# Optimization experiments

Measured on AMD Instinct MI355X. Metric: run time of the kernel, lower is better.

The kernel has to match this reference:

```python
import jax, jax.numpy as jnp
import numpy as np

# Geometry constants matching __init__ defaults
DG = 2        # deformable_groups
KS = 3        # kernel_size
K = KS * KS   # taps per kernel
DIL = 2       # dilation
PAD = 2       # padding = dilation
STRIDE = 1


def setup_inputs() -> dict:
    key = jax.random.key(0)
    k1, k2, k3, k4 = jax.random.split(key, 4)
    B, C, H, W = 4, 128, 96, 192
    Cout = 128
    x = jax.random.normal(k1, (B, C, H, W), dtype=jnp.float32)
    # offset/mask conv: grouped conv, groups=DG -> in-channels per group = C//DG
    off_out = DG * 3 * K  # 54 (36 offset + 18 mask)
    # small weights so learned offsets are O(1) pixels (realistic trained regime;
    # the original zero-init would make the gather trivial)
    w_offset = jax.random.normal(k2, (off_out, C // DG, KS, KS), dtype=jnp.float32) * 0.01
    b_offset = jax.random.normal(k3, (off_out,), dtype=jnp.float32) * 0.1
    stdv = 1.0 / np.sqrt(C * KS * KS)
    w_deform = jax.random.uniform(k4, (Cout, C, KS, KS), dtype=jnp.float32,
                                  minval=-stdv, maxval=stdv)
    return {"x": x, "w_offset": w_offset, "b_offset": b_offset, "w_deform": w_deform}


def _deform_conv2d(x, w_offset, b_offset, w_deform):
    B, C, H, W = x.shape
    Cout = w_deform.shape[0]
    Cg = C // DG
    # --- offset/mask conv (grouped, dilated) ---
    om = jax.lax.conv_general_dilated(
        x, w_offset, (STRIDE, STRIDE), [(PAD, PAD), (PAD, PAD)],
        rhs_dilation=(DIL, DIL), feature_group_count=DG,
        dimension_numbers=("NCHW", "OIHW", "NCHW"))
    om = om + b_offset[None, :, None, None]
    Ho, Wo = om.shape[2], om.shape[3]
    off_ch = DG * 2 * K
    offset = om[:, :off_ch]                       # [B, 36, Ho, Wo]
    mask = jax.nn.sigmoid(om[:, off_ch:]) * 2.0   # double_mask=True -> *2
    # torchvision layout: channel 2*(g*K+k) = dy, +1 = dx
    off = offset.reshape(B, DG, K, 2, Ho, Wo)
    m = mask.reshape(B, DG, K, Ho, Wo)
    # --- sampling coordinates ---
    ky = (jnp.arange(K) // KS).astype(x.dtype)
    kx = (jnp.arange(K) % KS).astype(x.dtype)
    base_y = (jnp.arange(Ho) * STRIDE - PAD).astype(x.dtype)
    base_x = (jnp.arange(Wo) * STRIDE - PAD).astype(x.dtype)
    py = base_y[None, None, None, :, None] + (ky * DIL)[None, None, :, None, None] + off[:, :, :, 0]
    px = base_x[None, None, None, None, :] + (kx * DIL)[None, None, :, None, None] + off[:, :, :, 1]
    y0 = jnp.floor(py)
    x0 = jnp.floor(px)
    ty = py - y0
    tx = px - x0
    xflat = x.reshape(B, DG, Cg, H * W)
    # gather[b,g,c,n] = xflat[b,g,c, idx[b,g,n]]
    gather = jax.vmap(jax.vmap(lambda xg, idx: jnp.take(xg, idx, axis=1)))
    val = jnp.zeros((B, DG, Cg, K, Ho, Wo), x.dtype)
    # accumulate bilinear corners one at a time to bound peak memory
    for dy, dx, wgt in ((0, 0, (1 - ty) * (1 - tx)), (0, 1, (1 - ty) * tx),
                        (1, 0, ty * (1 - tx)), (1, 1, ty * tx)):
        yy = y0 + dy
        xx = x0 + dx
        valid = (yy >= 0) & (yy < H) & (xx >= 0) & (xx < W)
        yc = jnp.clip(yy, 0, H - 1).astype(jnp.int32)
        xc = jnp.clip(xx, 0, W - 1).astype(jnp.int32)
        lin = (yc * W + xc).reshape(B, DG, K * Ho * Wo)
        g = gather(xflat, lin).reshape(B, DG, Cg, K, Ho, Wo)
        val = val + jnp.where(valid, wgt, 0.0)[:, :, None] * g
    val = val * m[:, :, None]  # modulation mask per deformable group / tap
    wr = w_deform.reshape(Cout, DG, Cg, K)
    return jnp.einsum("ogck,bgckhw->bohw", wr, val)


def reference(x, w_offset, b_offset, w_deform):
    return _deform_conv2d(x, w_offset, b_offset, w_deform)
```

## Files before the change

kernel.cpp:

```cpp
#include <hip/hip_runtime.h>
#include <hip/hip_fp16.h>
#include <math.h>

#define BB   4
#define C_   128
#define H_   96
#define W_   192
#define COUT 128
#define DG_  2
#define CG_  64
#define K_   9
#define HO   96
#define WO   192
#define HW   (H_ * W_)
#define OMCH 54
#define RDIM (C_ * K_)
#define NKS  (RDIM / 32)
#define CSTEP 2
#define NCH  (NKS / CSTEP)
#define VROW 18

typedef __attribute__((ext_vector_type(8))) _Float16 f16x8;
typedef __attribute__((ext_vector_type(4))) float f32x4;

static __device__ __forceinline__ ushort f2bf(float f) {
  union { float f; uint u; } v; v.f = f;
  uint r = v.u + 0x7fff + ((v.u >> 16) & 1);
  return (ushort)(r >> 16);
}

__global__ __launch_bounds__(256) void prep_k(
    const float* __restrict__ wd, const float* __restrict__ wo,
    ushort* __restrict__ WtA, ushort* __restrict__ Awo2) {
  int i = blockIdx.x * 256 + threadIdx.x;
  if (i < 128 * RDIM) {
    int blkA = i >> 9, within = i & 511;
    int oct = within >> 7, colA = (within >> 3) & 15, j = within & 7;
    int m = blkA & 1, wvq = (blkA >> 1) & 3, s = blkA >> 3;
    int o = wvq * 32 + m * 16 + colA;
    int r = s * 32 + oct * 8 + j;
    int g = r / 576, t = r - g * 576;
    int k = t >> 6, cg = t & 63;
    WtA[i] = __half_as_ushort(__float2half(wd[((size_t)o * C_ + g * 64 + cg) * 9 + k]));
  }
  if (i < 64 * RDIM) {
    int blkA = i >> 9, within = i & 511;
    int oct = within >> 7, colA = (within >> 3) & 15, j = within & 7;
    int wv2 = blkA & 3, s = blkA >> 2;
    int o2 = wv2 * 16 + colA;
    int r = s * 32 + oct * 8 + j;
    int g = r / 576, t = r - g * 576;
    int k = t >> 6, cg = t & 63;
    int g2 = o2 >> 5, j2 = o2 & 31;
    float v = ((g2 == g) && (j2 < 27))
                ? wo[(((size_t)(g2 * 27 + j2)) * 64 + cg) * 9 + k] : 0.f;
    Awo2[i] = __half_as_ushort(__float2half(v));
  }
}

__global__ __launch_bounds__(256) void xt_k(
    const float* __restrict__ x, __half* __restrict__ xT) {
  __shared__ float t[128][65];
  int blk = blockIdx.x;
  int b = blk / 288, p0 = (blk % 288) * 64;
  int q = threadIdx.x >> 6, l = threadIdx.x & 63;
  const float* xb = x + (size_t)b * C_ * HW;
#pragma unroll
  for (int it = 0; it < 32; ++it) {
    int c = q * 32 + it;
    t[c][l] = xb[(size_t)c * HW + p0 + l];
  }
  __syncthreads();
  uint* xTb = (uint*)(xT + (size_t)b * HW * 128);
#pragma unroll
  for (int it = 0; it < 16; ++it) {
    int px = q * 16 + it;
    union { __half2 h; uint u; } pk;
    pk.h = __half2{__float2half(t[2 * l][px]), __float2half(t[2 * l + 1][px])};
    xTb[(size_t)(p0 + px) * 64 + l] = pk.u;
  }
}

__global__ __launch_bounds__(256, 6) void offset_nhwc_k(
    const __half* __restrict__ xT, const ushort* __restrict__ Awo2,
    const float* __restrict__ b_offset, float* __restrict__ om) {
  __shared__ uint s_val[2][CSTEP * 64 * VROW];

  int bid = blockIdx.x;
  int blk = (bid & 7) * 144 + (bid >> 3);
  int wt = blk % 3, bh = blk / 3;
  int ho = bh % HO, b = bh / HO;
  int wo0 = wt * 64;
  int tid = threadIdx.x;
  int lane = tid & 63, wv = tid >> 6;
  int sub = lane >> 3, q = lane & 7;
  int col = lane & 15, oct = lane >> 4;

  const __half* xTb = xT + (size_t)b * HW * 128;

  f32x4 acc[4];
#pragma unroll
  for (int n = 0; n < 4; ++n) acc[n] = (f32x4){0.f, 0.f, 0.f, 0.f};

  uint4 C0[2];
  uint  MK[2];
  int   IX[2];

  auto issue_chunk = [&](int c) {
#pragma unroll
    for (int t = 0; t < 2; ++t) {
      int po = wv * 2 + t;
      int gk = c;
      int px = po * 8 + sub;
      int g = gk >= 9, k = gk - 9 * g;
      int dy = k / 3, dx = k - dy * 3;
      int y  = ho - 2 + 2 * dy;
      int xc = wo0 + px - 2 + 2 * dx;
      bool ok = (y >= 0) & (y < H_) & (xc >= 0) & (xc < W_);
      int yc  = min(max(y, 0), H_ - 1);
      int xcc = min(max(xc, 0), W_ - 1);
      const __half* p = xTb + (size_t)(yc * W_ + xcc) * 128 + g * 64 + q * 8;
      C0[t] = *(const uint4*)(p);
      MK[t] = ok ? 0x3c003c00u : 0u;
      int step_local = q >> 2;
      IX[t] = (step_local * 64 + px) * VROW + (q & 3) * 4;
    }
  };

  auto finish_chunk = [&](int nb) {
#pragma unroll
    for (int t = 0; t < 2; ++t) {
      union { __half2 h2; uint u; } m; m.u = MK[t];
      uint res[4];
      const uint* a = (const uint*)&C0[t];
#pragma unroll
      for (int h = 0; h < 4; ++h) {
        union { __half2 h2; uint u; } p, vv;
        p.u = a[h];
        vv.h2 = __hmul2(p.h2, m.h2);
        res[h] = vv.u;
      }
      *(uint4*)&s_val[nb][IX[t]] = make_uint4(res[0], res[1], res[2], res[3]);
    }
  };

  auto mfma_chunk = [&](int c, int cb) {
#pragma unroll
    for (int ls = 0; ls < CSTEP; ++ls) {
      int s = c * CSTEP + ls;
      const ushort* ab = Awo2 + (size_t)(s * 4 + wv) * 512 + (oct * 16 + col) * 8;
      f16x8 a0 = *(const f16x8*)(ab);
#pragma unroll
      for (int n = 0; n < 4; ++n) {
        f16x8 bfr = *(const f16x8*)
            &s_val[cb][(ls * 64 + n * 16 + col) * VROW + oct * 4];
        acc[n] = __builtin_amdgcn_mfma_f32_16x16x32_f16(a0, bfr, acc[n], 0, 0, 0);
      }
    }
  };

  issue_chunk(0);
  finish_chunk(0);
  __syncthreads();

  for (int c = 0; c < NCH; ++c) {
    if (c < NCH - 1) issue_chunk(c + 1);
    mfma_chunk(c, c & 1);
    if (c < NCH - 1) finish_chunk((c + 1) & 1);
    __syncthreads();
  }

#pragma unroll
  for (int n = 0; n < 4; ++n)
#pragma unroll
    for (int ri = 0; ri < 4; ++ri) {
      int o2 = wv * 16 + oct * 4 + ri;
      int g = o2 >> 5, j = o2 & 31;
      if (j < 27) {
        int ch = g * 27 + j;
        om[((size_t)(b * OMCH + ch) * HO + ho) * WO + wo0 + n * 16 + col] =
            acc[n][ri] + b_offset[ch];
      }
    }
}

__global__ __launch_bounds__(256, 4) void deform_main_k(
    const __half* __restrict__ xT, const float* __restrict__ om,
    const ushort* __restrict__ WtA, float* __restrict__ out) {
  __shared__ uint  s_addr[18 * 64];
  __shared__ uint2 s_wq[18 * 64];
  __shared__ uint  s_val[2][CSTEP * 64 * VROW];

  int bid = blockIdx.x;
  int blk = (bid & 7) * 144 + (bid >> 3);
  int wt = blk % 3, bh = blk / 3;
  int ho = bh % HO, b = bh / HO;
  int wo0 = wt * 64;
  int tid = threadIdx.x;
  int lane = tid & 63, wv = tid >> 6;

  for (int e = tid; e < 18 * 64; e += 256) {
    int px = e & 63, gk = e >> 6;
    int g = gk / 9, k = gk - g * 9;
    int wo = wo0 + px;
    const float* omb = om + (size_t)b * OMCH * HW + (size_t)ho * WO + wo;
    float offy = omb[(size_t)(g * 18 + k * 2 + 0) * HW];
    float offx = omb[(size_t)(g * 18 + k * 2 + 1) * HW];
    float z    = omb[(size_t)(36 + g * 9 + k) * HW];
    float msk  = 2.f / (1.f + __expf(-z));
    float py = (float)(ho - 2 + (k / 3) * 2) + offy;
    float px_ = (float)(wo - 2 + (k % 3) * 2) + offx;
    float y0f = floorf(py), x0f = floorf(px_);
    int   y0 = (int)y0f, x0 = (int)x0f;
    float ty = py - y0f, tx = px_ - x0f;
    float wy0 = (y0 >= 0 && y0 < H_)      ? (1.f - ty) : 0.f;
    float wy1 = (y0 >= -1 && y0 < H_ - 1) ? ty         : 0.f;
    float wx0 = (x0 >= 0 && x0 < W_)      ? (1.f - tx) : 0.f;
    float wx1 = (x0 >= -1 && x0 < W_ - 1) ? tx         : 0.f;
    int yb  = min(max(y0, 0), H_ - 2);
    int xb_ = min(max(x0, 0), W_ - 2);
    float wAy = (y0 == yb      ? wy0 : 0.f) + (y0 + 1 == yb      ? wy1 : 0.f);
    float wBy = (y0 == yb + 1  ? wy0 : 0.f) + (y0 + 1 == yb + 1  ? wy1 : 0.f);
    float wAx = (x0 == xb_     ? wx0 : 0.f) + (x0 + 1 == xb_     ? wx1 : 0.f);
    float wBx = (x0 == xb_ + 1 ? wx0 : 0.f) + (x0 + 1 == xb_ + 1 ? wx1 : 0.f);
    s_addr[e] = (uint)((yb * W_ + xb_) * 128);
    union { __half2 h; uint u; } uA, uB;
    uA.h = __half2{__float2half(wAy * wAx * msk), __float2half(wAy * wBx * msk)};
    uB.h = __half2{__float2half(wBy * wAx * msk), __float2half(wBy * wBx * msk)};
    s_wq[e] = make_uint2(uA.u, uB.u);
  }

  const __half* xTb = xT + (size_t)b * HW * 128;
  int sub = lane >> 3, q = lane & 7;
  int col = lane & 15, oct = lane >> 4;

  f32x4 acc[2][4];
#pragma unroll
  for (int m = 0; m < 2; ++m)
#pragma unroll
    for (int n = 0; n < 4; ++n) acc[m][n] = (f32x4){0.f, 0.f, 0.f, 0.f};

  uint4 C0[2], C1[2], C2[2], C3[2];
  uint2 WQ[2];
  int   IX[2];

  auto issue_chunk = [&](int c) {
#pragma unroll
    for (int t = 0; t < 2; ++t) {
      int po = wv * 2 + t;
      int gk = c;
      int px = po * 8 + sub;
      int ci = gk * 64 + px;
      uint base = s_addr[ci];
      WQ[t] = s_wq[ci];
      int g = gk >= 9;
      const __half* p = xTb + base + g * 64 + q * 8;
      C0[t] = *(const uint4*)(p);
      C1[t] = *(const uint4*)(p + 128);
      C2[t] = *(const uint4*)(p + W_ * 128);
      C3[t] = *(const uint4*)(p + W_ * 128 + 128);
      int step_local = q >> 2;
      int row = step_local * 64 + px;
      IX[t] = row * VROW + (q & 3) * 4;
    }
  };

  auto finish_chunk = [&](int nb) {
#pragma unroll
    for (int t = 0; t < 2; ++t) {
      union { __half2 h; uint u; } w0, w1;
      w0.u = WQ[t].x; w1.u = WQ[t].y;
      __half2 wAx = __low2half2(w0.h), wAy = __high2half2(w0.h);
      __half2 wBx = __low2half2(w1.h), wBy = __high2half2(w1.h);
      uint res[4];
      const uint* a  = (const uint*)&C0[t];
      const uint* b1 = (const uint*)&C1[t];
      const uint* c2 = (const uint*)&C2[t];
      const uint* d  = (const uint*)&C3[t];
#pragma unroll
      for (int h = 0; h < 4; ++h) {
        union { __half2 h2; uint u; } p0, p1, p2, p3, vv;
        p0.u = a[h]; p1.u = b1[h]; p2.u = c2[h]; p3.u = d[h];
        __half2 v = __hmul2(p0.h2, wAx);
        v = __hfma2(p1.h2, wAy, v);
        v = __hfma2(p2.h2, wBx, v);
        v = __hfma2(p3.h2, wBy, v);
        vv.h2 = v;
        res[h] = vv.u;
      }
      *(uint4*)&s_val[nb][IX[t]] = make_uint4(res[0], res[1], res[2], res[3]);
    }
  };

  auto mfma_chunk = [&](int c, int cb) {
#pragma unroll
    for (int ls = 0; ls < CSTEP; ++ls) {
      int s = c * CSTEP + ls;
      const ushort* ab = WtA + (size_t)((s * 4 + wv) * 2) * 512 + (oct * 16 + col) * 8;
      f16x8 a0 = *(const f16x8*)(ab);
      f16x8 a1 = *(const f16x8*)(ab + 512);
#pragma unroll
      for (int n = 0; n < 4; ++n) {
        f16x8 bfr = *(const f16x8*)
            &s_val[cb][(ls * 64 + n * 16 + col) * VROW + oct * 4];
        acc[0][n] = __builtin_amdgcn_mfma_f32_16x16x32_f16(a0, bfr, acc[0][n], 0, 0, 0);
        acc[1][n] = __builtin_amdgcn_mfma_f32_16x16x32_f16(a1, bfr, acc[1][n], 0, 0, 0);
      }
    }
  };

  __syncthreads();
  issue_chunk(0);
  finish_chunk(0);
  __syncthreads();

  for (int c = 0; c < NCH; ++c) {
    if (c < NCH - 1) issue_chunk(c + 1);
    mfma_chunk(c, c & 1);
    if (c < NCH - 1) finish_chunk((c + 1) & 1);
    __syncthreads();
  }

#pragma unroll
  for (int m = 0; m < 2; ++m)
#pragma unroll
    for (int n = 0; n < 4; ++n)
#pragma unroll
      for (int ri = 0; ri < 4; ++ri) {
        int o = wv * 32 + m * 16 + oct * 4 + ri;
        out[((size_t)(b * COUT + o) * HO + ho) * WO + wo0 + n * 16 + col] = acc[m][n][ri];
      }
}

extern "C" void kernel_launch(void* const* d_in, const int* in_sizes, int n_in,
                              void* d_out, int out_size, void* d_ws, size_t ws_size,
                              hipStream_t stream) {
  const float* x        = (const float*)d_in[0];
  const float* w_offset = (const float*)d_in[1];
  const float* b_offset = (const float*)d_in[2];
  const float* w_deform = (const float*)d_in[3];
  float* out = (float*)d_out;

  char* ws = (char*)d_ws;
  float*  om   = (float*)ws;
  ushort* WtA  = (ushort*)(ws + 15925248);
  ushort* Awo2 = (ushort*)(ws + 15925248 + 294912);
  __half* xT   = (__half*)(ws + 15925248 + 294912 + 147456);

  prep_k<<<576, 256, 0, stream>>>(w_deform, w_offset, WtA, Awo2);
  xt_k<<<1152, 256, 0, stream>>>(x, xT);
  offset_nhwc_k<<<1152, 256, 0, stream>>>(xT, Awo2, b_offset, om);
  deform_main_k<<<1152, 256, 0, stream>>>(xT, om, WtA, out);
}
```

Measured before the change: 92.19 us.

## Deepen gather pipeline to two chunks in flight with triple-buffered LDS

Both the offset conv and the main deformable kernel now keep two chunks of global gathers in flight, using register double-buffering plus a third shared-memory buffer. The aim is to hide more gather latency behind the MFMA work. In exchange, register and LDS use go up, so the launch-bounds occupancy targets drop (6→5 and 4→3). That may reduce latency hiding across waves.

```diff
diff --git a/kernel.cpp b/kernel.cpp
--- a/kernel.cpp
+++ b/kernel.cpp
@@ -81,10 +81,10 @@
   }
 }
 
-__global__ __launch_bounds__(256, 6) void offset_nhwc_k(
+__global__ __launch_bounds__(256, 5) void offset_nhwc_k(
     const __half* __restrict__ xT, const ushort* __restrict__ Awo2,
     const float* __restrict__ b_offset, float* __restrict__ om) {
-  __shared__ uint s_val[2][CSTEP * 64 * VROW];
+  __shared__ uint s_val[3][CSTEP * 64 * VROW];
 
   int bid = blockIdx.x;
   int blk = (bid & 7) * 144 + (bid >> 3);
@@ -102,11 +102,11 @@
 #pragma unroll
   for (int n = 0; n < 4; ++n) acc[n] = (f32x4){0.f, 0.f, 0.f, 0.f};
 
-  uint4 C0[2];
-  uint  MK[2];
-  int   IX[2];
-
-  auto issue_chunk = [&](int c) {
+  uint4 A0[2], B0[2];
+  uint  MKa[2], MKb[2];
+  int   IXa[2], IXb[2];
+
+  auto issue = [&](int c, uint4 (&K0)[2], uint (&MK)[2], int (&IX)[2]) {
 #pragma unroll
     for (int t = 0; t < 2; ++t) {
       int po = wv * 2 + t;
@@ -120,19 +120,19 @@
       int yc  = min(max(y, 0), H_ - 1);
       int xcc = min(max(xc, 0), W_ - 1);
       const __half* p = xTb + (size_t)(yc * W_ + xcc) * 128 + g * 64 + q * 8;
-      C0[t] = *(const uint4*)(p);
+      K0[t] = *(const uint4*)(p);
       MK[t] = ok ? 0x3c003c00u : 0u;
-      int step_local = q >> 2;
-      IX[t] = (step_local * 64 + px) * VROW + (q & 3) * 4;
-    }
-  };
-
-  auto finish_chunk = [&](int nb) {
+      IX[t] = ((q >> 2) * 64 + px) * VROW + (q & 3) * 4;
+    }
+  };
+
+  auto finish = [&](int nb, const uint4 (&K0)[2], const uint (&MK)[2],
+                    const int (&IX)[2]) {
 #pragma unroll
     for (int t = 0; t < 2; ++t) {
       union { __half2 h2; uint u; } m; m.u = MK[t];
       uint res[4];
-      const uint* a = (const uint*)&C0[t];
+      const uint* a = (const uint*)&K0[t];
 #pragma unroll
       for (int h = 0; h < 4; ++h) {
         union { __half2 h2; uint u; } p, vv;
@@ -159,15 +159,24 @@
     }
   };
 
-  issue_chunk(0);
-  finish_chunk(0);
+  issue(0, A0, MKa, IXa);
+  issue(1, B0, MKb, IXb);
+  finish(0, A0, MKa, IXa);
   __syncthreads();
 
-  for (int c = 0; c < NCH; ++c) {
-    if (c < NCH - 1) issue_chunk(c + 1);
-    mfma_chunk(c, c & 1);
-    if (c < NCH - 1) finish_chunk((c + 1) & 1);
-    __syncthreads();
+  for (int c2 = 0; c2 < NCH; c2 += 2) {
+    { int c = c2;
+      if (c + 2 < NCH) issue(c + 2, A0, MKa, IXa);
+      mfma_chunk(c, c % 3);
+      finish((c + 1) % 3, B0, MKb, IXb);
+      __syncthreads();
+    }
+    { int c = c2 + 1;
+      if (c + 2 < NCH) issue(c + 2, B0, MKb, IXb);
+      mfma_chunk(c, c % 3);
+      if (c + 1 < NCH) finish((c + 1) % 3, A0, MKa, IXa);
+      __syncthreads();
+    }
   }
 
 #pragma unroll
@@ -184,12 +193,12 @@
     }
 }
 
-__global__ __launch_bounds__(256, 4) void deform_main_k(
+__global__ __launch_bounds__(256, 3) void deform_main_k(
     const __half* __restrict__ xT, const float* __restrict__ om,
     const ushort* __restrict__ WtA, float* __restrict__ out) {
   __shared__ uint  s_addr[18 * 64];
   __shared__ uint2 s_wq[18 * 64];
-  __shared__ uint  s_val[2][CSTEP * 64 * VROW];
+  __shared__ uint  s_val[3][CSTEP * 64 * VROW];
 
   int bid = blockIdx.x;
   int blk = (bid & 7) * 144 + (bid >> 3);
@@ -240,11 +249,13 @@
 #pragma unroll
     for (int n = 0; n < 4; ++n) acc[m][n] = (f32x4){0.f, 0.f, 0.f, 0.f};
 
-  uint4 C0[2], C1[2], C2[2], C3[2];
-  uint2 WQ[2];
-  int   IX[2];
-
-  auto issue_chunk = [&](int c) {
+  uint4 A0[2], A1[2], A2[2], A3[2];
+  uint4 B0[2], B1[2], B2[2], B3[2];
+  uint2 WQa[2], WQb[2];
+  int   IXa[2], IXb[2];
+
+  auto issue = [&](int c, uint4 (&K0)[2], uint4 (&K1)[2], uint4 (&K2)[2],
+                   uint4 (&K3)[2], uint2 (&WQ)[2], int (&IX)[2]) {
 #pragma unroll
     for (int t = 0; t < 2; ++t) {
       int po = wv * 2 + t;
@@ -255,17 +266,17 @@
       WQ[t] = s_wq[ci];
       int g = gk >= 9;
       const __half* p = xTb + base + g * 64 + q * 8;
-      C0[t] = *(const uint4*)(p);
-      C1[t] = *(const uint4*)(p + 128);
-      C2[t] = *(const uint4*)(p + W_ * 128);
-      C3[t] = *(const uint4*)(p + W_ * 128 + 128);
-      int step_local = q >> 2;
-      int row = step_local * 64 + px;
-      IX[t] = row * VROW + (q & 3) * 4;
-    }
-  };
-
-  auto finish_chunk = [&](int nb) {
+      K0[t] = *(const uint4*)(p);
+      K1[t] = *(const uint4*)(p + 128);
+      K2[t] = *(const uint4*)(p + W_ * 128);
+      K3[t] = *(const uint4*)(p + W_ * 128 + 128);
+      IX[t] = ((q >> 2) * 64 + px) * VROW + (q & 3) * 4;
+    }
+  };
+
+  auto finish = [&](int nb, const uint4 (&K0)[2], const uint4 (&K1)[2],
+                    const uint4 (&K2)[2], const uint4 (&K3)[2],
+                    const uint2 (&WQ)[2], const int (&IX)[2]) {
 #pragma unroll
     for (int t = 0; t < 2; ++t) {
       union { __half2 h; uint u; } w0, w1;
@@ -273,10 +284,10 @@
       __half2 wAx = __low2half2(w0.h), wAy = __high2half2(w0.h);
       __half2 wBx = __low2half2(w1.h), wBy = __high2half2(w1.h);
       uint res[4];
-      const uint* a  = (const uint*)&C0[t];
-      const uint* b1 = (const uint*)&C1[t];
-      const uint* c2 = (const uint*)&C2[t];
-      const uint* d  = (const uint*)&C3[t];
+      const uint* a  = (const uint*)&K0[t];
+      const uint* b1 = (const uint*)&K1[t];
+      const uint* c2 = (const uint*)&K2[t];
+      const uint* d  = (const uint*)&K3[t];
 #pragma unroll
       for (int h = 0; h < 4; ++h) {
         union { __half2 h2; uint u; } p0, p1, p2, p3, vv;
@@ -310,15 +321,24 @@
   };
 
   __syncthreads();
-  issue_chunk(0);
-  finish_chunk(0);
+  issue(0, A0, A1, A2, A3, WQa, IXa);
+  issue(1, B0, B1, B2, B3, WQb, IXb);
+  finish(0, A0, A1, A2, A3, WQa, IXa);
   __syncthreads();
 
-  for (int c = 0; c < NCH; ++c) {
-    if (c < NCH - 1) issue_chunk(c + 1);
-    mfma_chunk(c, c & 1);
-    if (c < NCH - 1) finish_chunk((c + 1) & 1);
-    __syncthreads();
+  for (int c2 = 0; c2 < NCH; c2 += 2) {
+    { int c = c2;
+      if (c + 2 < NCH) issue(c + 2, A0, A1, A2, A3, WQa, IXa);
+      mfma_chunk(c, c % 3);
+      finish((c + 1) % 3, B0, B1, B2, B3, WQb, IXb);
+      __syncthreads();
+    }
+    { int c = c2 + 1;
+      if (c + 2 < NCH) issue(c + 2, B0, B1, B2, B3, WQb, IXb);
+      mfma_chunk(c, c % 3);
+      if (c + 1 < NCH) finish((c + 1) % 3, A0, A1, A2, A3, WQa, IXa);
+      __syncthreads();
+    }
   }
 
 #pragma unroll
```

After: 96.24 us. +4.4%, slower.
